# Performance work log

Measured on AMD Instinct MI355X. Metric: run time of the kernel, lower is better.

Reference implementation:

```python
import jax, jax.numpy as jnp
import numpy as np

D_E = 128
D_R = 128  # must equal D_E for the original torch code to typecheck
BN_EPS = 1e-5


def setup_inputs() -> dict:
    key = jax.random.key(0)
    ks = jax.random.split(key, 8)
    B, S = 16, 2048
    h = jax.random.normal(ks[0], (B, S, D_E), dtype=jnp.float32)
    r = jax.random.normal(ks[1], (B, S, D_R), dtype=jnp.float32)
    t = jax.random.normal(ks[2], (B, S, D_E), dtype=jnp.float32)
    # Xavier-uniform core tensor W: (d_r, d_e, d_e)
    limit = float(np.sqrt(6.0 / (D_R + D_E * D_E)))
    W = jax.random.uniform(ks[3], (D_R, D_E, D_E), minval=-limit, maxval=limit, dtype=jnp.float32)
    # BatchNorm1d params/buffers (inference mode)
    gamma0 = jnp.ones((D_E,), jnp.float32)
    beta0 = jnp.zeros((D_E,), jnp.float32)
    mean0 = 0.1 * jax.random.normal(ks[4], (D_E,), dtype=jnp.float32)
    var0 = jnp.abs(1.0 + 0.1 * jax.random.normal(ks[5], (D_E,), dtype=jnp.float32))
    gamma1 = jnp.ones((D_E,), jnp.float32)
    beta1 = jnp.zeros((D_E,), jnp.float32)
    mean1 = 0.1 * jax.random.normal(ks[6], (D_E,), dtype=jnp.float32)
    var1 = jnp.abs(1.0 + 0.1 * jax.random.normal(ks[7], (D_E,), dtype=jnp.float32))
    return {"h": h, "r": r, "t": t, "W": W,
            "gamma0": gamma0, "beta0": beta0, "mean0": mean0, "var0": var0,
            "gamma1": gamma1, "beta1": beta1, "mean1": mean1, "var1": var1}


def reference(h, r, t, W, gamma0, beta0, mean0, var0, gamma1, beta1, mean1, var1):
    B, S, D = h.shape  # D == d_e == d_r
    N = B * S
    # BatchNorm1d in eval mode over last dim; dropout is identity in eval.
    h_bn = (h - mean0) * jax.lax.rsqrt(var0 + BN_EPS) * gamma0 + beta0
    t_bn = (t - mean1) * jax.lax.rsqrt(var1 + BN_EPS) * gamma1 + beta1
    r2 = r.reshape(N, D)
    # torch.matmul((N,d_r), (d_r,d_e,d_e)) broadcasts -> shape (d_r, N, d_e):
    #   out[k, n, j] = sum_i r2[n, i] * W[k, i, j]
    # followed by .view(N, d_e, d_e) which reinterprets the flat buffer.
    W_mat = jnp.einsum('ni,kij->knj', r2, W).reshape(N, D, D)  # (N, d_e, d_e) after scrambled view
    # hr[n, j] = sum_d h_bn[n, d] * W_mat[n, d, j]
    hr = jnp.einsum('nd,ndj->nj', h_bn.reshape(N, D), W_mat)
    scores = jnp.sum(hr * t_bn.reshape(N, D), axis=-1)  # (N,)
    return scores.reshape(B, S)
```

## Files before the change

kernel.cpp:

```cpp
#include <hip/hip_runtime.h>


typedef __attribute__((ext_vector_type(8))) short bf16x8;
typedef __attribute__((ext_vector_type(4))) short s16x4;
typedef __attribute__((ext_vector_type(4))) float f32x4;

#define DPAD 136
#define BN_EPS 1e-5f

__device__ inline unsigned short f2bf(float f) {
  unsigned u = __builtin_bit_cast(unsigned, f);
  u += 0x7FFFu + ((u >> 16) & 1u);
  return (unsigned short)(u >> 16);
}
__device__ inline float bf2f(unsigned short h) {
  unsigned u = ((unsigned)h) << 16;
  return __builtin_bit_cast(float, u);
}

__global__ __launch_bounds__(256) void k_stageA(
    const float* __restrict__ t, const float* __restrict__ W,
    const float* __restrict__ gamma1, const float* __restrict__ beta1,
    const float* __restrict__ mean1, const float* __restrict__ var1,
    unsigned short* __restrict__ V) {
  __shared__ short Tl[128 * DPAD];
  __shared__ short Wl[128 * DPAD];
  const int tid = threadIdx.x;
  const int k = blockIdx.x >> 1;
  const int half = blockIdx.x & 1;
  const int rowbase = k * 256 + half * 128;

  const int c = tid & 31;
  const int rr = tid >> 5;
  f32x4 g  = *(const f32x4*)(gamma1 + c * 4);
  f32x4 be = *(const f32x4*)(beta1  + c * 4);
  f32x4 mu = *(const f32x4*)(mean1  + c * 4);
  f32x4 va = *(const f32x4*)(var1   + c * 4);
  f32x4 sc, bi;
  for (int q = 0; q < 4; ++q) {
    sc[q] = g[q] * rsqrtf(va[q] + BN_EPS);
    bi[q] = be[q] - mu[q] * sc[q];
  }
  const float* tbase = t + (size_t)rowbase * 128;
  const float* wbase = W + (size_t)k * 16384;
  for (int it = 0; it < 16; ++it) {
    const int m = it * 8 + rr;
    f32x4 tv = *(const f32x4*)(tbase + m * 128 + c * 4);
    s16x4 tb;
    for (int q = 0; q < 4; ++q) tb[q] = (short)f2bf(tv[q] * sc[q] + bi[q]);
    *(s16x4*)(&Tl[m * DPAD + c * 4]) = tb;
    f32x4 wv = *(const f32x4*)(wbase + m * 128 + c * 4);
    s16x4 wb;
    for (int q = 0; q < 4; ++q) wb[q] = (short)f2bf(wv[q]);
    *(s16x4*)(&Wl[m * DPAD + c * 4]) = wb;
  }
  __syncthreads();

  const int wv_ = tid >> 6;
  const int lane = tid & 63;
  const int l16 = lane & 15;
  const int quad = lane >> 4;
  f32x4 acc[2][8];
  for (int mt = 0; mt < 2; ++mt)
    for (int nt = 0; nt < 8; ++nt) acc[mt][nt] = (f32x4){0.f, 0.f, 0.f, 0.f};

  for (int ks = 0; ks < 4; ++ks) {
    const int K0 = ks * 32 + quad * 8;
    bf16x8 a[2], b[8];
    for (int mt = 0; mt < 2; ++mt)
      a[mt] = *(const bf16x8*)(&Tl[(wv_ * 32 + mt * 16 + l16) * DPAD + K0]);
    for (int nt = 0; nt < 8; ++nt)
      b[nt] = *(const bf16x8*)(&Wl[(nt * 16 + l16) * DPAD + K0]);
    for (int mt = 0; mt < 2; ++mt)
      for (int nt = 0; nt < 8; ++nt)
        acc[mt][nt] = __builtin_amdgcn_mfma_f32_16x16x32_bf16(a[mt], b[nt], acc[mt][nt], 0, 0, 0);
  }

  for (int mt = 0; mt < 2; ++mt) {
    const int rbase2 = rowbase + wv_ * 32 + mt * 16 + quad * 4;
    for (int nt = 0; nt < 8; ++nt) {
      const int col = nt * 16 + l16;
      for (int rg = 0; rg < 4; ++rg)
        V[(size_t)(rbase2 + rg) * 128 + col] = f2bf(acc[mt][nt][rg]);
    }
  }
}

__global__ __launch_bounds__(256) void k_stageB(
    const float* __restrict__ h, const float* __restrict__ r,
    const float* __restrict__ gamma0, const float* __restrict__ beta0,
    const float* __restrict__ mean0, const float* __restrict__ var0,
    unsigned short* __restrict__ U) {
  __shared__ short Hl[128 * DPAD];
  __shared__ short Rl[128 * DPAD];
  const int tid = threadIdx.x;
  const int low = blockIdx.x;

  const int c = tid & 31;
  const int rr = tid >> 5;
  f32x4 g  = *(const f32x4*)(gamma0 + c * 4);
  f32x4 be = *(const f32x4*)(beta0  + c * 4);
  f32x4 mu = *(const f32x4*)(mean0  + c * 4);
  f32x4 va = *(const f32x4*)(var0   + c * 4);
  f32x4 sc, bi;
  for (int q = 0; q < 4; ++q) {
    sc[q] = g[q] * rsqrtf(va[q] + BN_EPS);
    bi[q] = be[q] - mu[q] * sc[q];
  }
  for (int it = 0; it < 16; ++it) {
    const int kk = it * 8 + rr;
    f32x4 hv = *(const f32x4*)(h + ((size_t)(kk * 256 + low)) * 128 + c * 4);
    s16x4 hb;
    for (int q = 0; q < 4; ++q) hb[q] = (short)f2bf(hv[q] * sc[q] + bi[q]);
    *(s16x4*)(&Hl[kk * DPAD + c * 4]) = hb;
  }
  for (int it = 0; it < 4; ++it) {
    const int a0 = it * 32 + rr * 4;
    f32x4 rv[4];
    for (int v = 0; v < 4; ++v)
      rv[v] = *(const f32x4*)(r + ((size_t)(low * 128 + a0 + v)) * 128 + c * 4);
    for (int u = 0; u < 4; ++u) {
      s16x4 w;
      for (int v = 0; v < 4; ++v) w[v] = (short)f2bf(rv[v][u]);
      *(s16x4*)(&Rl[(c * 4 + u) * DPAD + a0]) = w;
    }
  }
  __syncthreads();

  const int wv_ = tid >> 6;
  const int lane = tid & 63;
  const int l16 = lane & 15;
  const int quad = lane >> 4;
  f32x4 acc[2][8];
  for (int mt = 0; mt < 2; ++mt)
    for (int nt = 0; nt < 8; ++nt) acc[mt][nt] = (f32x4){0.f, 0.f, 0.f, 0.f};

  for (int ks = 0; ks < 4; ++ks) {
    const int K0 = ks * 32 + quad * 8;
    bf16x8 a[2], b[8];
    for (int mt = 0; mt < 2; ++mt)
      a[mt] = *(const bf16x8*)(&Hl[(wv_ * 32 + mt * 16 + l16) * DPAD + K0]);
    for (int nt = 0; nt < 8; ++nt)
      b[nt] = *(const bf16x8*)(&Rl[(nt * 16 + l16) * DPAD + K0]);
    for (int mt = 0; mt < 2; ++mt)
      for (int nt = 0; nt < 8; ++nt)
        acc[mt][nt] = __builtin_amdgcn_mfma_f32_16x16x32_bf16(a[mt], b[nt], acc[mt][nt], 0, 0, 0);
  }

  for (int mt = 0; mt < 2; ++mt) {
    const int kkbase = wv_ * 32 + mt * 16 + quad * 4;
    for (int nt = 0; nt < 8; ++nt) {
      const int col = nt * 16 + l16;
      for (int rg = 0; rg < 4; ++rg)
        U[(size_t)((kkbase + rg) * 256 + low) * 128 + col] = f2bf(acc[mt][nt][rg]);
    }
  }
}

__global__ __launch_bounds__(256) void k_dot(
    const unsigned short* __restrict__ U, const unsigned short* __restrict__ V,
    float* __restrict__ out) {
  const int tid = threadIdx.x;
  const int row = blockIdx.x * 16 + (tid >> 4);
  const int l = tid & 15;
  const uint4 uv = *(const uint4*)(U + (size_t)row * 128 + l * 8);
  const uint4 vv = *(const uint4*)(V + (size_t)row * 128 + l * 8);
  const unsigned* up = (const unsigned*)&uv;
  const unsigned* vp = (const unsigned*)&vv;
  float s = 0.f;
  for (int q = 0; q < 4; ++q) {
    unsigned a = up[q], b = vp[q];
    s += bf2f((unsigned short)(a & 0xFFFFu)) * bf2f((unsigned short)(b & 0xFFFFu));
    s += bf2f((unsigned short)(a >> 16)) * bf2f((unsigned short)(b >> 16));
  }
  for (int m = 1; m < 16; m <<= 1) s += __shfl_xor(s, m, 16);
  if (l == 0) out[row] = s;
}

extern "C" void kernel_launch(void* const* d_in, const int* in_sizes, int n_in,
                              void* d_out, int out_size, void* d_ws, size_t ws_size,
                              hipStream_t stream) {
  const float* h      = (const float*)d_in[0];
  const float* r      = (const float*)d_in[1];
  const float* t      = (const float*)d_in[2];
  const float* W      = (const float*)d_in[3];
  const float* gamma0 = (const float*)d_in[4];
  const float* beta0  = (const float*)d_in[5];
  const float* mean0  = (const float*)d_in[6];
  const float* var0   = (const float*)d_in[7];
  const float* gamma1 = (const float*)d_in[8];
  const float* beta1  = (const float*)d_in[9];
  const float* mean1  = (const float*)d_in[10];
  const float* var1   = (const float*)d_in[11];
  float* out = (float*)d_out;

  unsigned short* V = (unsigned short*)d_ws;
  unsigned short* U = V + (size_t)32768 * 128;

  k_stageA<<<256, 256, 0, stream>>>(t, W, gamma1, beta1, mean1, var1, V);
  k_stageB<<<256, 256, 0, stream>>>(h, r, gamma0, beta0, mean0, var0, U);
  k_dot<<<2048, 256, 0, stream>>>(U, V, out);
}
```

Before: 118.9 us.

## Merge two GEMM stages into one launch and vectorize transposed output stores

Combines the two independent per-row GEMM kernels into a single 512-block launch, with blockIdx selecting the branch, so both stages run concurrently and fill the GPU. It also swaps the MFMA operand order so each lane holds 4 contiguous output columns, which lets results be packed and stored as 8-byte writes instead of scattered 2-byte stores. The cost is one launch boundary fewer, in exchange for branch-divergent register and shared-memory use within a single kernel.

```diff
diff --git a/kernel.cpp b/kernel.cpp
--- a/kernel.cpp
+++ b/kernel.cpp
@@ -17,142 +17,134 @@
   unsigned u = ((unsigned)h) << 16;
   return __builtin_bit_cast(float, u);
 }
+__device__ inline unsigned pack2bf(float lo, float hi) {
+  return (unsigned)f2bf(lo) | ((unsigned)f2bf(hi) << 16);
+}
 
-__global__ __launch_bounds__(256) void k_stageA(
+__global__ __launch_bounds__(256) void k_uv(
+    const float* __restrict__ h, const float* __restrict__ r,
     const float* __restrict__ t, const float* __restrict__ W,
+    const float* __restrict__ gamma0, const float* __restrict__ beta0,
+    const float* __restrict__ mean0, const float* __restrict__ var0,
     const float* __restrict__ gamma1, const float* __restrict__ beta1,
     const float* __restrict__ mean1, const float* __restrict__ var1,
-    unsigned short* __restrict__ V) {
-  __shared__ short Tl[128 * DPAD];
-  __shared__ short Wl[128 * DPAD];
+    unsigned short* __restrict__ V, unsigned short* __restrict__ U) {
+  __shared__ short LA[128 * DPAD];
+  __shared__ short LB[128 * DPAD];
   const int tid = threadIdx.x;
-  const int k = blockIdx.x >> 1;
-  const int half = blockIdx.x & 1;
-  const int rowbase = k * 256 + half * 128;
-
   const int c = tid & 31;
   const int rr = tid >> 5;
-  f32x4 g  = *(const f32x4*)(gamma1 + c * 4);
-  f32x4 be = *(const f32x4*)(beta1  + c * 4);
-  f32x4 mu = *(const f32x4*)(mean1  + c * 4);
-  f32x4 va = *(const f32x4*)(var1   + c * 4);
-  f32x4 sc, bi;
-  for (int q = 0; q < 4; ++q) {
-    sc[q] = g[q] * rsqrtf(va[q] + BN_EPS);
-    bi[q] = be[q] - mu[q] * sc[q];
-  }
-  const float* tbase = t + (size_t)rowbase * 128;
-  const float* wbase = W + (size_t)k * 16384;
-  for (int it = 0; it < 16; ++it) {
-    const int m = it * 8 + rr;
-    f32x4 tv = *(const f32x4*)(tbase + m * 128 + c * 4);
-    s16x4 tb;
-    for (int q = 0; q < 4; ++q) tb[q] = (short)f2bf(tv[q] * sc[q] + bi[q]);
-    *(s16x4*)(&Tl[m * DPAD + c * 4]) = tb;
-    f32x4 wv = *(const f32x4*)(wbase + m * 128 + c * 4);
-    s16x4 wb;
-    for (int q = 0; q < 4; ++q) wb[q] = (short)f2bf(wv[q]);
-    *(s16x4*)(&Wl[m * DPAD + c * 4]) = wb;
-  }
-  __syncthreads();
-
   const int wv_ = tid >> 6;
   const int lane = tid & 63;
   const int l16 = lane & 15;
   const int quad = lane >> 4;
+
   f32x4 acc[2][8];
   for (int mt = 0; mt < 2; ++mt)
     for (int nt = 0; nt < 8; ++nt) acc[mt][nt] = (f32x4){0.f, 0.f, 0.f, 0.f};
 
-  for (int ks = 0; ks < 4; ++ks) {
-    const int K0 = ks * 32 + quad * 8;
-    bf16x8 a[2], b[8];
-    for (int mt = 0; mt < 2; ++mt)
-      a[mt] = *(const bf16x8*)(&Tl[(wv_ * 32 + mt * 16 + l16) * DPAD + K0]);
-    for (int nt = 0; nt < 8; ++nt)
-      b[nt] = *(const bf16x8*)(&Wl[(nt * 16 + l16) * DPAD + K0]);
-    for (int mt = 0; mt < 2; ++mt)
+  if (blockIdx.x < 256) {
+    const int k = blockIdx.x >> 1;
+    const int half = blockIdx.x & 1;
+    const int rowbase = k * 256 + half * 128;
+
+    f32x4 g  = *(const f32x4*)(gamma1 + c * 4);
+    f32x4 be = *(const f32x4*)(beta1  + c * 4);
+    f32x4 mu = *(const f32x4*)(mean1  + c * 4);
+    f32x4 va = *(const f32x4*)(var1   + c * 4);
+    f32x4 sc, bi;
+    for (int q = 0; q < 4; ++q) {
+      sc[q] = g[q] * rsqrtf(va[q] + BN_EPS);
+      bi[q] = be[q] - mu[q] * sc[q];
+    }
+    const float* tbase = t + (size_t)rowbase * 128;
+    const float* wbase = W + (size_t)k * 16384;
+    for (int it = 0; it < 16; ++it) {
+      const int m = it * 8 + rr;
+      f32x4 tv = *(const f32x4*)(tbase + m * 128 + c * 4);
+      s16x4 tb;
+      for (int q = 0; q < 4; ++q) tb[q] = (short)f2bf(tv[q] * sc[q] + bi[q]);
+      *(s16x4*)(&LA[m * DPAD + c * 4]) = tb;
+      f32x4 wvv = *(const f32x4*)(wbase + m * 128 + c * 4);
+      s16x4 wb;
+      for (int q = 0; q < 4; ++q) wb[q] = (short)f2bf(wvv[q]);
+      *(s16x4*)(&LB[m * DPAD + c * 4]) = wb;
+    }
+    __syncthreads();
+
+    for (int ks = 0; ks < 4; ++ks) {
+      const int K0 = ks * 32 + quad * 8;
+      bf16x8 a[2], b[8];
+      for (int mt = 0; mt < 2; ++mt)
+        a[mt] = *(const bf16x8*)(&LA[(wv_ * 32 + mt * 16 + l16) * DPAD + K0]);
       for (int nt = 0; nt < 8; ++nt)
-        acc[mt][nt] = __builtin_amdgcn_mfma_f32_16x16x32_bf16(a[mt], b[nt], acc[mt][nt], 0, 0, 0);
-  }
+        b[nt] = *(const bf16x8*)(&LB[(nt * 16 + l16) * DPAD + K0]);
+      for (int mt = 0; mt < 2; ++mt)
+        for (int nt = 0; nt < 8; ++nt)
+          acc[mt][nt] = __builtin_amdgcn_mfma_f32_16x16x32_bf16(b[nt], a[mt], acc[mt][nt], 0, 0, 0);
+    }
 
-  for (int mt = 0; mt < 2; ++mt) {
-    const int rbase2 = rowbase + wv_ * 32 + mt * 16 + quad * 4;
-    for (int nt = 0; nt < 8; ++nt) {
-      const int col = nt * 16 + l16;
-      for (int rg = 0; rg < 4; ++rg)
-        V[(size_t)(rbase2 + rg) * 128 + col] = f2bf(acc[mt][nt][rg]);
+    for (int mt = 0; mt < 2; ++mt) {
+      const size_t np = (size_t)(rowbase + wv_ * 32 + mt * 16 + l16) * 128;
+      for (int nt = 0; nt < 8; ++nt) {
+        unsigned two[2];
+        two[0] = pack2bf(acc[mt][nt][0], acc[mt][nt][1]);
+        two[1] = pack2bf(acc[mt][nt][2], acc[mt][nt][3]);
+        *(uint2*)(V + np + nt * 16 + quad * 4) = *(uint2*)two;
+      }
     }
-  }
-}
+  } else {
+    const int low = blockIdx.x - 256;
 
-__global__ __launch_bounds__(256) void k_stageB(
-    const float* __restrict__ h, const float* __restrict__ r,
-    const float* __restrict__ gamma0, const float* __restrict__ beta0,
-    const float* __restrict__ mean0, const float* __restrict__ var0,
-    unsigned short* __restrict__ U) {
-  __shared__ short Hl[128 * DPAD];
-  __shared__ short Rl[128 * DPAD];
-  const int tid = threadIdx.x;
-  const int low = blockIdx.x;
+    f32x4 g  = *(const f32x4*)(gamma0 + c * 4);
+    f32x4 be = *(const f32x4*)(beta0  + c * 4);
+    f32x4 mu = *(const f32x4*)(mean0  + c * 4);
+    f32x4 va = *(const f32x4*)(var0   + c * 4);
+    f32x4 sc, bi;
+    for (int q = 0; q < 4; ++q) {
+      sc[q] = g[q] * rsqrtf(va[q] + BN_EPS);
+      bi[q] = be[q] - mu[q] * sc[q];
+    }
+    for (int it = 0; it < 16; ++it) {
+      const int kk = it * 8 + rr;
+      f32x4 hv = *(const f32x4*)(h + ((size_t)(kk * 256 + low)) * 128 + c * 4);
+      s16x4 hb;
+      for (int q = 0; q < 4; ++q) hb[q] = (short)f2bf(hv[q] * sc[q] + bi[q]);
+      *(s16x4*)(&LA[kk * DPAD + c * 4]) = hb;
+    }
+    for (int it = 0; it < 4; ++it) {
+      const int a0 = it * 32 + rr * 4;
+      f32x4 rv[4];
+      for (int v = 0; v < 4; ++v)
+        rv[v] = *(const f32x4*)(r + ((size_t)(low * 128 + a0 + v)) * 128 + c * 4);
+      for (int u = 0; u < 4; ++u) {
+        s16x4 w;
+        for (int v = 0; v < 4; ++v) w[v] = (short)f2bf(rv[v][u]);
+        *(s16x4*)(&LB[(c * 4 + u) * DPAD + a0]) = w;
+      }
+    }
+    __syncthreads();
 
-  const int c = tid & 31;
-  const int rr = tid >> 5;
-  f32x4 g  = *(const f32x4*)(gamma0 + c * 4);
-  f32x4 be = *(const f32x4*)(beta0  + c * 4);
-  f32x4 mu = *(const f32x4*)(mean0  + c * 4);
-  f32x4 va = *(const f32x4*)(var0   + c * 4);
-  f32x4 sc, bi;
-  for (int q = 0; q < 4; ++q) {
-    sc[q] = g[q] * rsqrtf(va[q] + BN_EPS);
-    bi[q] = be[q] - mu[q] * sc[q];
-  }
-  for (int it = 0; it < 16; ++it) {
-    const int kk = it * 8 + rr;
-    f32x4 hv = *(const f32x4*)(h + ((size_t)(kk * 256 + low)) * 128 + c * 4);
-    s16x4 hb;
-    for (int q = 0; q < 4; ++q) hb[q] = (short)f2bf(hv[q] * sc[q] + bi[q]);
-    *(s16x4*)(&Hl[kk * DPAD + c * 4]) = hb;
-  }
-  for (int it = 0; it < 4; ++it) {
-    const int a0 = it * 32 + rr * 4;
-    f32x4 rv[4];
-    for (int v = 0; v < 4; ++v)
-      rv[v] = *(const f32x4*)(r + ((size_t)(low * 128 + a0 + v)) * 128 + c * 4);
-    for (int u = 0; u < 4; ++u) {
-      s16x4 w;
-      for (int v = 0; v < 4; ++v) w[v] = (short)f2bf(rv[v][u]);
-      *(s16x4*)(&Rl[(c * 4 + u) * DPAD + a0]) = w;
+    for (int ks = 0; ks < 4; ++ks) {
+      const int K0 = ks * 32 + quad * 8;
+      bf16x8 a[2], b[8];
+      for (int mt = 0; mt < 2; ++mt)
+        a[mt] = *(const bf16x8*)(&LA[(wv_ * 32 + mt * 16 + l16) * DPAD + K0]);
+      for (int nt = 0; nt < 8; ++nt)
+        b[nt] = *(const bf16x8*)(&LB[(nt * 16 + l16) * DPAD + K0]);
+      for (int mt = 0; mt < 2; ++mt)
+        for (int nt = 0; nt < 8; ++nt)
+          acc[mt][nt] = __builtin_amdgcn_mfma_f32_16x16x32_bf16(b[nt], a[mt], acc[mt][nt], 0, 0, 0);
     }
-  }
-  __syncthreads();
 
-  const int wv_ = tid >> 6;
-  const int lane = tid & 63;
-  const int l16 = lane & 15;
-  const int quad = lane >> 4;
-  f32x4 acc[2][8];
-  for (int mt = 0; mt < 2; ++mt)
-    for (int nt = 0; nt < 8; ++nt) acc[mt][nt] = (f32x4){0.f, 0.f, 0.f, 0.f};
-
-  for (int ks = 0; ks < 4; ++ks) {
-    const int K0 = ks * 32 + quad * 8;
-    bf16x8 a[2], b[8];
-    for (int mt = 0; mt < 2; ++mt)
-      a[mt] = *(const bf16x8*)(&Hl[(wv_ * 32 + mt * 16 + l16) * DPAD + K0]);
-    for (int nt = 0; nt < 8; ++nt)
-      b[nt] = *(const bf16x8*)(&Rl[(nt * 16 + l16) * DPAD + K0]);
-    for (int mt = 0; mt < 2; ++mt)
-      for (int nt = 0; nt < 8; ++nt)
-        acc[mt][nt] = __builtin_amdgcn_mfma_f32_16x16x32_bf16(a[mt], b[nt], acc[mt][nt], 0, 0, 0);
-  }
-
-  for (int mt = 0; mt < 2; ++mt) {
-    const int kkbase = wv_ * 32 + mt * 16 + quad * 4;
-    for (int nt = 0; nt < 8; ++nt) {
-      const int col = nt * 16 + l16;
-      for (int rg = 0; rg < 4; ++rg)
-        U[(size_t)((kkbase + rg) * 256 + low) * 128 + col] = f2bf(acc[mt][nt][rg]);
+    for (int mt = 0; mt < 2; ++mt) {
+      const size_t np = ((size_t)(wv_ * 32 + mt * 16 + l16) * 256 + low) * 128;
+      for (int nt = 0; nt < 8; ++nt) {
+        unsigned two[2];
+        two[0] = pack2bf(acc[mt][nt][0], acc[mt][nt][1]);
+        two[1] = pack2bf(acc[mt][nt][2], acc[mt][nt][3]);
+        *(uint2*)(U + np + nt * 16 + quad * 4) = *(uint2*)two;
+      }
     }
   }
 }
@@ -197,7 +189,8 @@
   unsigned short* V = (unsigned short*)d_ws;
   unsigned short* U = V + (size_t)32768 * 128;
 
-  k_stageA<<<256, 256, 0, stream>>>(t, W, gamma1, beta1, mean1, var1, V);
-  k_stageB<<<256, 256, 0, stream>>>(h, r, gamma0, beta0, mean0, var0, U);
+  k_uv<<<512, 256, 0, stream>>>(h, r, t, W,
+                                gamma0, beta0, mean0, var0,
+                                gamma1, beta1, mean1, var1, V, U);
   k_dot<<<2048, 256, 0, stream>>>(U, V, out);
 }
```

Result: no change. 116.8 us (-1.8%).
